# Optimization experiments

Measured on AMD Instinct MI355X. Metric: run time of the kernel, lower is better.

The kernel has to match this reference:

```python
import jax, jax.numpy as jnp
import numpy as np

W_DIM = 512
NF = 128          # n_features (all blocks equal)
NB = 4            # num_layers / n_blocks
B = 8             # batch
INIT = 32         # initial resolution: 2**(8 - 4 + 1)
IMG = 256         # 2**log_resolution
EPS = 1e-8


def setup_inputs() -> dict:
    key = jax.random.key(0)
    ks = jax.random.split(key, 12)
    d = {}
    d["w"] = jax.random.normal(ks[0], (NB, B, W_DIM), jnp.float32)
    for i in range(NB):
        r = INIT * (2 ** i)
        d[f"noise{i}"] = jax.random.normal(ks[1 + i], (2, B, 1, r, r), jnp.float32)
    # learned parameters
    d["initial_constant"] = jax.random.normal(ks[5], (1, NF, INIT, INIT), jnp.float32)
    d["to_style_w"] = jax.random.normal(ks[6], (NB, NF, W_DIM), jnp.float32)      # EqualizedLinear weights
    d["to_style_b"] = 0.1 * jax.random.normal(ks[7], (NB, NF), jnp.float32)
    d["conv_w"] = jax.random.normal(ks[8], (NB, 2, NF, NF, 3, 3), jnp.float32)    # two StyleBlock convs per block
    d["scale_noise"] = 0.1 * jax.random.normal(ks[9], (NB, 2), jnp.float32)
    d["style_bias"] = 0.1 * jax.random.normal(ks[10], (NB, 2, NF), jnp.float32)
    d["rgb_w"] = jax.random.normal(ks[11], (NB, 1, NF, 1, 1), jnp.float32)        # ToRGB 1x1 convs
    return d


def _resize(x, h, w):
    # bilinear, half-pixel centers (matches F.interpolate align_corners=False)
    return jax.image.resize(x, (x.shape[0], x.shape[1], h, w), "bilinear")


def _mod_conv(x, s, weight, demodulate):
    # x: [B, Cin, H, W], s: [B, Cin], weight: [Cout, Cin, k, k]
    out_c, in_c, k, _ = weight.shape
    c = 1.0 / np.sqrt(in_c * k * k)  # EqualizedWeight scale
    ws = (weight * c)[None] * s[:, None, :, None, None]  # [B, Cout, Cin, k, k]
    if demodulate:
        ws = ws * jax.lax.rsqrt(jnp.sum(ws * ws, axis=(2, 3, 4), keepdims=True) + EPS)
    conv = lambda xi, wi: jax.lax.conv_general_dilated(xi[None], wi, (1, 1), "SAME")[0]
    return jax.vmap(conv)(x, ws)  # per-sample weights == grouped conv with groups=B


def _style_block(x, s, wconv, sn, b, noise):
    x = _mod_conv(x, s, wconv, True)
    x = x + sn * noise
    return jax.nn.leaky_relu(x + b[None, :, None, None], 0.2)


def reference(w, noise0, noise1, noise2, noise3, initial_constant, to_style_w,
              to_style_b, conv_w, scale_noise, style_bias, rgb_w):
    noises = [noise0, noise1, noise2, noise3]
    b = w.shape[1]
    x = jax.nn.relu(jnp.broadcast_to(initial_constant, (b,) + initial_constant.shape[1:]))
    cl = 1.0 / np.sqrt(W_DIM)  # EqualizedLinear scale
    rgb_sum = jnp.zeros((b, 1, IMG, IMG), x.dtype)
    for i in range(NB):
        if i > 0:
            x = _resize(x, x.shape[2] * 2, x.shape[3] * 2)
        s = w[i] @ (to_style_w[i] * cl).T + to_style_b[i]  # [B, NF]
        x = _style_block(x, s, conv_w[i, 0], scale_noise[i, 0], style_bias[i, 0], noises[i][0])
        x = _style_block(x, s, conv_w[i, 1], scale_noise[i, 1], style_bias[i, 1], noises[i][1])
        rgb = _mod_conv(x, s, rgb_w[i], False)  # [B, 1, h, w]
        rgb_sum = rgb_sum + _resize(rgb, IMG, IMG)
    return rgb_sum / 2 + 0.5
```

## Files before the change

kernel.cpp:

```cpp
#include <hip/hip_runtime.h>
#include <math.h>

#define NB 4
#define BATCH 8
#define NF 128
#define WDIM 512
#define EPS_D 1e-8f

typedef unsigned short ushortT;
typedef __attribute__((ext_vector_type(8))) short short8v;
typedef __attribute__((ext_vector_type(8))) unsigned short ushort8v;
typedef __attribute__((ext_vector_type(4))) float float4v;
typedef __attribute__((ext_vector_type(4))) unsigned int uint4v;
typedef __attribute__((ext_vector_type(2))) unsigned int uint2v;

__device__ inline unsigned short f2bf(float f) {
    unsigned u = __builtin_bit_cast(unsigned, f);
    u = (u + 0x7fffu + ((u >> 16) & 1u)) >> 16;
    return (unsigned short)u;
}
__device__ inline float bf2f(unsigned short h) {
    unsigned u = ((unsigned)h) << 16;
    return __builtin_bit_cast(float, u);
}

__global__ void k_style(const float* __restrict__ w,
                        const float* __restrict__ tsw,
                        const float* __restrict__ tsb,
                        float* __restrict__ s) {
    int gid = blockIdx.x * blockDim.x + threadIdx.x;
    if (gid >= NB * BATCH * NF) return;
    int i = gid >> 10;
    int b = (gid >> 7) & 7;
    int o = gid & 127;
    const float cl = 0.044194173824159216f;
    const float* wr = w + (i * BATCH + b) * WDIM;
    const float* tr = tsw + (i * NF + o) * WDIM;
    float acc = 0.f;
    for (int k = 0; k < WDIM; ++k) acc += wr[k] * tr[k];
    s[gid] = acc * cl + tsb[i * NF + o];
}

__global__ void k_demod(const float* __restrict__ conv_w,
                        const float* __restrict__ s,
                        float* __restrict__ d) {
    int bx = blockIdx.x;
    int l = bx >> 7;
    int o = bx & 127;
    int lane = threadIdx.x;
    const float* wb = conv_w + (size_t)((l * NF + o) * NF) * 9;
    float t0 = 0.f, t1 = 0.f;
    for (int k = 0; k < 9; ++k) {
        float a = wb[lane * 9 + k];        t0 += a * a;
        float c = wb[(lane + 64) * 9 + k]; t1 += c * c;
    }
    const float c2 = 1.0f / 1152.0f;
    int i = l >> 1;
    for (int b = 0; b < BATCH; ++b) {
        float s0 = s[(i * BATCH + b) * NF + lane];
        float s1 = s[(i * BATCH + b) * NF + lane + 64];
        float v = t0 * s0 * s0 + t1 * s1 * s1;
        for (int off = 32; off > 0; off >>= 1) v += __shfl_down(v, off);
        if (lane == 0) d[(l * BATCH + b) * NF + o] = rsqrtf(v * c2 + EPS_D);
    }
}

__global__ void k_wmodF(const float* __restrict__ cw, const float* __restrict__ s,
                        ushortT* __restrict__ wm) {
    int idx = blockIdx.x * blockDim.x + threadIdx.x;
    int lane = idx & 63;
    int mf = (idx >> 6) & 7;
    int kcc = (idx >> 9) & 3;
    int t = (idx >> 11) % 9;
    int r2 = idx / (2048 * 9);
    int b = r2 & 7;
    int l = r2 >> 3;
    if (l >= 8) return;
    const float cscale = 0.029462782549439483f;
    int co = mf * 16 + (lane & 15);
    int kb = kcc * 32 + (lane >> 4) * 8;
    const float* src = cw + (((size_t)l * NF + co) * NF) * 9;
    const float* sr = s + ((l >> 1) * BATCH + b) * NF;
    ushort8v o;
    #pragma unroll
    for (int e = 0; e < 8; ++e) {
        int ci = kb + e;
        o[e] = f2bf(src[(size_t)ci * 9 + t] * cscale * sr[ci]);
    }
    *(ushort8v*)(wm + (size_t)idx * 8) = o;
}

__global__ void k_prep_init(const float* __restrict__ ic, ushortT* __restrict__ xp,
                            int total) {
    for (int idx = blockIdx.x * blockDim.x + threadIdx.x; idx < total;
         idx += gridDim.x * blockDim.x) {
        int ci = idx & 127;
        int p = (idx >> 7) & 1023;
        float v = ic[ci * 1024 + p];
        xp[idx] = f2bf(v > 0.f ? v : 0.f);
    }
}

__global__ void k_up2_bf(const ushortT* __restrict__ in, ushortT* __restrict__ out,
                         int h, int w, int total) {
    int W2 = w * 2, H2 = h * 2;
    for (int gid = blockIdx.x * blockDim.x + threadIdx.x; gid < total;
         gid += gridDim.x * blockDim.x) {
        int cg = gid & 15;
        int t = gid >> 4;
        int ox = t % W2; t /= W2;
        int oy = t % H2; int zb = t / H2;
        int y0 = (oy >> 1) - 1 + (oy & 1);
        float wy0 = (oy & 1) ? 0.75f : 0.25f;
        int x0 = (ox >> 1) - 1 + (ox & 1);
        float wx0 = (ox & 1) ? 0.75f : 0.25f;
        int y1 = min(y0 + 1, h - 1); y0 = max(y0, 0);
        int x1 = min(x0 + 1, w - 1); x0 = max(x0, 0);
        const ushortT* base = in + (size_t)zb * h * w * 128 + cg * 8;
        ushort8v v00 = *(const ushort8v*)(base + (size_t)(y0 * w + x0) * 128);
        ushort8v v01 = *(const ushort8v*)(base + (size_t)(y0 * w + x1) * 128);
        ushort8v v10 = *(const ushort8v*)(base + (size_t)(y1 * w + x0) * 128);
        ushort8v v11 = *(const ushort8v*)(base + (size_t)(y1 * w + x1) * 128);
        float wy1 = 1.f - wy0, wx1 = 1.f - wx0;
        ushort8v o;
        #pragma unroll
        for (int k = 0; k < 8; ++k) {
            float v = wy0 * (wx0 * bf2f(v00[k]) + wx1 * bf2f(v01[k]))
                    + wy1 * (wx0 * bf2f(v10[k]) + wx1 * bf2f(v11[k]));
            o[k] = f2bf(v);
        }
        *(ushort8v*)(out + ((size_t)(zb * H2 + oy) * W2 + ox) * 128 + cg * 8) = o;
    }
}

template<int NOY>
__global__ __launch_bounds__(256, 3) void k_conv7(
    const ushortT* __restrict__ xp, ushortT* __restrict__ yp,
    const ushortT* __restrict__ wF, const float* __restrict__ d_b,
    const float* __restrict__ nz, const float* __restrict__ bias,
    const float* __restrict__ sn_ptr, const float* __restrict__ s_blk,
    const float* __restrict__ rgbw_i, float* __restrict__ rgbb,
    int H, int W, int b0, int do_rgb)
{
    __shared__ __align__(16) char lb[46080];
    int tid = threadIdx.x;
    int lane = tid & 63;
    int wv = tid >> 6;
    int wm = wv & 1, wn = wv >> 1;
    int lm = lane & 15, lk = lane >> 4;
    int tilesX = W >> 4;
    int tx0 = (blockIdx.x % tilesX) << 4;
    int ty0 = (blockIdx.x / tilesX) << 3;
    int zb = blockIdx.y;
    int b = b0 + zb;

    const char* xbase = (const char*)(xp + (size_t)zb * H * W * 128);
    int offs[6];
    #pragma unroll
    for (int it = 0; it < 6; ++it) {
        int cw = it * 64 + lane;
        int off = -1;
        if (cw < 360) {
            int chunk = wv * 360 + cw;
            int px = chunk >> 3, slot = chunk & 7;
            int hy = px / 18, hx = px - hy * 18;
            int gy = ty0 + hy - 1, gx = tx0 + hx - 1;
            if ((unsigned)gy < (unsigned)H && (unsigned)gx < (unsigned)W)
                off = (gy * W + gx) * 256 + ((slot ^ (px & 7)) << 4);
        }
        offs[it] = off;
    }
    {
        const uint4v zv = {0, 0, 0, 0};
        #pragma unroll
        for (int c = 0; c < 12; ++c) {
            int idx = tid + c * 256;
            if (idx < 2880) *(uint4v*)(lb + idx * 16) = zv;
        }
    }
    __syncthreads();
    #pragma unroll
    for (int it = 0; it < 6; ++it)
        if (offs[it] >= 0)
            __builtin_amdgcn_global_load_lds(
                (const __attribute__((address_space(1))) void*)(xbase + offs[it]),
                (__attribute__((address_space(3))) void*)(lb + wv * 5760 + it * 1024), 16, 0, 0);
    __syncthreads();
    #pragma unroll
    for (int it = 0; it < 6; ++it)
        if (offs[it] >= 0)
            __builtin_amdgcn_global_load_lds(
                (const __attribute__((address_space(1))) void*)(xbase + offs[it] + 128),
                (__attribute__((address_space(3))) void*)(lb + 23040 + wv * 5760 + it * 1024), 16, 0, 0);

    float4v acc[4][4];
    #pragma unroll
    for (int mf = 0; mf < 4; ++mf)
        #pragma unroll
        for (int nf = 0; nf < 4; ++nf)
            acc[mf][nf] = (float4v){0.f, 0.f, 0.f, 0.f};

    const ushortT* wB = wF + (size_t)b * (9 * 4 * 4096);
    for (int cih = 0; cih < 2; ++cih) {
        if (cih) __syncthreads();
        const char* buf = lb + cih * 23040;
        #pragma unroll
        for (int tap = 0; tap < 9; ++tap) {
            const int dy = (tap < 3) ? 0 : (tap < 6 ? 1 : 2);
            const int dx = tap - dy * 3;
            #pragma unroll
            for (int kc = 0; kc < 2; ++kc) {
                const ushortT* ap = wB + ((size_t)(tap * 4 + cih * 2 + kc) << 12)
                                    + wm * 2048 + lane * 8;
                short8v a0 = *(const short8v*)(ap);
                short8v a1 = *(const short8v*)(ap + 512);
                short8v a2 = *(const short8v*)(ap + 1024);
                short8v a3 = *(const short8v*)(ap + 1536);
                #pragma unroll
                for (int nf = 0; nf < 4; ++nf) {
                    int row = nf * 2 + (lm >> 3) + dy;
                    int col = wn * 8 + (lm & 7) + dx;
                    int hp = row * 18 + col;
                    short8v bf = *(const short8v*)(buf + hp * 128
                                 + ((((kc << 2) + lk) ^ (hp & 7)) << 4));
                    acc[0][nf] = __builtin_amdgcn_mfma_f32_16x16x32_bf16(a0, bf, acc[0][nf], 0, 0, 0);
                    acc[1][nf] = __builtin_amdgcn_mfma_f32_16x16x32_bf16(a1, bf, acc[1][nf], 0, 0, 0);
                    acc[2][nf] = __builtin_amdgcn_mfma_f32_16x16x32_bf16(a2, bf, acc[2][nf], 0, 0, 0);
                    acc[3][nf] = __builtin_amdgcn_mfma_f32_16x16x32_bf16(a3, bf, acc[3][nf], 0, 0, 0);
                }
            }
        }
    }
    __syncthreads();

    float sn = sn_ptr[0];
    float nv[4];
    #pragma unroll
    for (int nf = 0; nf < 4; ++nf) {
        int gy = ty0 + nf * 2 + (lm >> 3);
        int gx = tx0 + wn * 8 + (lm & 7);
        nv[nf] = sn * nz[((size_t)b * H + gy) * W + gx];
    }
    const float cl2 = 0.08838834764831845f;

    if (NOY) {
        float rgbs[4] = {0.f, 0.f, 0.f, 0.f};
        #pragma unroll
        for (int mf = 0; mf < 4; ++mf) {
            int co0 = wm * 64 + mf * 16 + lk * 4;
            float4v dd = *(const float4v*)(d_b + b * 128 + co0);
            float4v bb = *(const float4v*)(bias + co0);
            float4v rw = *(const float4v*)(rgbw_i + co0);
            float4v sv = *(const float4v*)(s_blk + b * 128 + co0);
            #pragma unroll
            for (int nf = 0; nf < 4; ++nf)
                #pragma unroll
                for (int e = 0; e < 4; ++e) {
                    float t = acc[mf][nf][e] * dd[e] + nv[nf] + bb[e];
                    t = t > 0.f ? t : 0.2f * t;
                    rgbs[nf] += t * rw[e] * cl2 * sv[e];
                }
        }
        #pragma unroll
        for (int nf = 0; nf < 4; ++nf) {
            float r = rgbs[nf];
            r += __shfl_xor(r, 16, 64);
            r += __shfl_xor(r, 32, 64);
            if (lane < 16) {
                int gy = ty0 + nf * 2 + (lane >> 3);
                int gx = tx0 + wn * 8 + (lane & 7);
                rgbb[((size_t)(wm * BATCH + b) * H + gy) * W + gx] = r;
            }
        }
        return;
    }

    float rgbs[4] = {0.f, 0.f, 0.f, 0.f};
    unsigned pka[4][4][2];
    #pragma unroll
    for (int mf = 0; mf < 4; ++mf) {
        int co0 = wm * 64 + mf * 16 + lk * 4;
        float4v dd = *(const float4v*)(d_b + b * 128 + co0);
        float4v bb = *(const float4v*)(bias + co0);
        float4v cf = {0.f, 0.f, 0.f, 0.f};
        if (do_rgb) {
            float4v rw = *(const float4v*)(rgbw_i + co0);
            float4v sv = *(const float4v*)(s_blk + b * 128 + co0);
            #pragma unroll
            for (int e = 0; e < 4; ++e) cf[e] = rw[e] * cl2 * sv[e];
        }
        #pragma unroll
        for (int nf = 0; nf < 4; ++nf) {
            float v[4];
            #pragma unroll
            for (int e = 0; e < 4; ++e) {
                float t = acc[mf][nf][e] * dd[e] + nv[nf] + bb[e];
                v[e] = t > 0.f ? t : 0.2f * t;
            }
            if (do_rgb)
                rgbs[nf] += v[0] * cf[0] + v[1] * cf[1] + v[2] * cf[2] + v[3] * cf[3];
            pka[mf][nf][0] = (unsigned)f2bf(v[0]) | ((unsigned)f2bf(v[1]) << 16);
            pka[mf][nf][1] = (unsigned)f2bf(v[2]) | ((unsigned)f2bf(v[3]) << 16);
        }
    }
    if (do_rgb) {
        #pragma unroll
        for (int nf = 0; nf < 4; ++nf) {
            float r = rgbs[nf];
            r += __shfl_xor(r, 16, 64);
            r += __shfl_xor(r, 32, 64);
            if (lane < 16) {
                int gy = ty0 + nf * 2 + (lane >> 3);
                int gx = tx0 + wn * 8 + (lane & 7);
                rgbb[((size_t)(wm * BATCH + b) * H + gy) * W + gx] = r;
            }
        }
    }
    char* xb2 = (char*)(yp + (size_t)zb * H * W * 128);
    #pragma unroll
    for (int h = 0; h < 2; ++h) {
        if (wm == h) {
            #pragma unroll
            for (int mf = 0; mf < 4; ++mf) {
                int cb = (mf * 16 + lk * 4) * 2;
                #pragma unroll
                for (int nf = 0; nf < 4; ++nf) {
                    int pxl = (nf * 2 + (lm >> 3)) * 16 + wn * 8 + (lm & 7);
                    int ad = pxl * 128 + (cb ^ ((pxl & 7) << 4));
                    uint2v pk2;
                    pk2[0] = pka[mf][nf][0];
                    pk2[1] = pka[mf][nf][1];
                    *(uint2v*)(lb + ad) = pk2;
                }
            }
        }
        __syncthreads();
        for (int c = tid; c < 1024; c += 256) {
            int pxl = c >> 3, ck = c & 7;
            uint4v v = *(const uint4v*)(lb + pxl * 128 + ((ck << 4) ^ ((pxl & 7) << 4)));
            int gy = ty0 + (pxl >> 4), gx = tx0 + (pxl & 15);
            *(uint4v*)(xb2 + ((size_t)(gy * W + gx)) * 256 + h * 128 + ck * 16) = v;
        }
        if (h == 0) __syncthreads();
    }
}

__global__ __launch_bounds__(256, 2) void k_mega(
    const ushortT* __restrict__ up256,
    const ushortT* __restrict__ wm6,
    const ushortT* __restrict__ wm7,
    const float* __restrict__ d6, const float* __restrict__ d7,
    const float* __restrict__ nz6, const float* __restrict__ nz7,
    const float* __restrict__ bias6, const float* __restrict__ bias7,
    const float* __restrict__ sn6p, const float* __restrict__ sn7p,
    const float* __restrict__ s_blk, const float* __restrict__ rgbw_i,
    float* __restrict__ rgbb, int b0)
{
    __shared__ __align__(16) char lb[61440];
    const int J0 = 15360;
    int tid = threadIdx.x;
    int lane = tid & 63;
    int wv = tid >> 6;
    int wm = wv & 1, wn = wv >> 1;
    int lm = lane & 15, lk = lane >> 4;
    int tx0 = (blockIdx.x & 15) << 4;
    int ty0 = (blockIdx.x >> 4) << 3;
    int zb = blockIdx.y;
    int b = b0 + zb;

    int ib[6], prr[6], pcc[6];
    bool pv[6];
    #pragma unroll
    for (int nf = 0; nf < 6; ++nf) {
        int p = wn * 96 + nf * 16 + lm;
        pv[nf] = (p < 180);
        int pc = pv[nf] ? p : 0;
        prr[nf] = pc / 18;
        pcc[nf] = pc - prr[nf] * 18;
        ib[nf] = prr[nf] * 20 + pcc[nf];
    }

    const char* xbase = (const char*)(up256 + (size_t)zb * 256 * 256 * 128);
    int offs[4];
    #pragma unroll
    for (int k = 0; k < 4; ++k) {
        int c = tid + k * 256;
        int off = -1;
        if (c < 960) {
            int ip = c >> 2, d = c & 3;
            int iy = ip / 20, ix = ip - iy * 20;
            int oy = ty0 + iy - 2, ox = tx0 + ix - 2;
            if ((unsigned)oy < 256u && (unsigned)ox < 256u)
                off = (oy * 256 + ox) * 256 + ((d ^ ((ip >> 1) & 3)) << 4);
        }
        offs[k] = off;
    }
    {
        const uint4v zv = {0, 0, 0, 0};
        for (int c = tid; c < 960; c += 256) *(uint4v*)(lb + c * 16) = zv;
    }
    __syncthreads();

    float4v j0a[4][6];
    #pragma unroll
    for (int mf = 0; mf < 4; ++mf)
        #pragma unroll
        for (int nf = 0; nf < 6; ++nf)
            j0a[mf][nf] = (float4v){0.f, 0.f, 0.f, 0.f};

    const ushortT* wB6 = wm6 + (size_t)b * (9 * 4 * 4096);
    const ushortT* wB7 = wm7 + (size_t)b * (9 * 4 * 4096);

    for (int q = 0; q < 4; ++q) {
        __builtin_amdgcn_sched_barrier(0);
        #pragma unroll
        for (int k = 0; k < 4; ++k)
            if (offs[k] >= 0)
                __builtin_amdgcn_global_load_lds(
                    (const __attribute__((address_space(1))) void*)(xbase + offs[k] + q * 64),
                    (__attribute__((address_space(3))) void*)(lb + k * 4096 + wv * 1024), 16, 0, 0);
        asm volatile("s_waitcnt vmcnt(0)" ::: "memory");
        __builtin_amdgcn_sched_barrier(0);
        __syncthreads();
        #pragma unroll
        for (int tap = 0; tap < 9; ++tap) {
            const int dy = (tap < 3) ? 0 : (tap < 6 ? 1 : 2);
            const int dx = tap - dy * 3;
            const ushortT* ap = wB6 + ((size_t)(tap * 4 + q) << 12) + wm * 2048 + lane * 8;
            short8v a0 = *(const short8v*)(ap);
            short8v a1 = *(const short8v*)(ap + 512);
            short8v a2 = *(const short8v*)(ap + 1024);
            short8v a3 = *(const short8v*)(ap + 1536);
            #pragma unroll
            for (int nf = 0; nf < 6; ++nf) {
                int ipx = ib[nf] + dy * 20 + dx;
                short8v bf = *(const short8v*)(lb + ipx * 64
                             + ((lk ^ ((ipx >> 1) & 3)) << 4));
                j0a[0][nf] = __builtin_amdgcn_mfma_f32_16x16x32_bf16(a0, bf, j0a[0][nf], 0, 0, 0);
                j0a[1][nf] = __builtin_amdgcn_mfma_f32_16x16x32_bf16(a1, bf, j0a[1][nf], 0, 0, 0);
                j0a[2][nf] = __builtin_amdgcn_mfma_f32_16x16x32_bf16(a2, bf, j0a[2][nf], 0, 0, 0);
                j0a[3][nf] = __builtin_amdgcn_mfma_f32_16x16x32_bf16(a3, bf, j0a[3][nf], 0, 0, 0);
            }
        }
        __builtin_amdgcn_sched_barrier(0);
        __syncthreads();
        __builtin_amdgcn_sched_barrier(0);
    }

    {
        float sn6 = sn6p[0];
        #pragma unroll
        for (int nf = 0; nf < 6; ++nf) {
            if (!pv[nf]) continue;
            int p = wn * 96 + nf * 16 + lm;
            int oy = ty0 + prr[nf] - 1, ox = tx0 + pcc[nf] - 1;
            bool inimg = ((unsigned)oy < 256u) && ((unsigned)ox < 256u);
            float nv = inimg ? sn6 * nz6[((size_t)b * 256 + oy) * 256 + ox] : 0.f;
            #pragma unroll
            for (int mf = 0; mf < 4; ++mf) {
                int co0 = wm * 64 + mf * 16 + lk * 4;
                uint2v pk2 = {0u, 0u};
                if (inimg) {
                    float4v dd = *(const float4v*)(d6 + b * 128 + co0);
                    float4v bb = *(const float4v*)(bias6 + co0);
                    float v[4];
                    #pragma unroll
                    for (int e = 0; e < 4; ++e) {
                        float t = j0a[mf][nf][e] * dd[e] + nv + bb[e];
                        v[e] = t > 0.f ? t : 0.2f * t;
                    }
                    pk2[0] = (unsigned)f2bf(v[0]) | ((unsigned)f2bf(v[1]) << 16);
                    pk2[1] = (unsigned)f2bf(v[2]) | ((unsigned)f2bf(v[3]) << 16);
                }
                int ad = p * 256 + ((co0 * 2) ^ ((p & 7) << 4));
                *(uint2v*)(lb + J0 + ad) = pk2;
            }
        }
    }
    __syncthreads();

    float4v acc[4][4];
    #pragma unroll
    for (int mf = 0; mf < 4; ++mf)
        #pragma unroll
        for (int nf = 0; nf < 4; ++nf)
            acc[mf][nf] = (float4v){0.f, 0.f, 0.f, 0.f};

    #pragma unroll
    for (int tap = 0; tap < 9; ++tap) {
        const int dy = (tap < 3) ? 0 : (tap < 6 ? 1 : 2);
        const int dx = tap - dy * 3;
        #pragma unroll
        for (int kcc = 0; kcc < 4; ++kcc) {
            const ushortT* ap = wB7 + ((size_t)(tap * 4 + kcc) << 12) + wm * 2048 + lane * 8;
            short8v a0 = *(const short8v*)(ap);
            short8v a1 = *(const short8v*)(ap + 512);
            short8v a2 = *(const short8v*)(ap + 1024);
            short8v a3 = *(const short8v*)(ap + 1536);
            #pragma unroll
            for (int nf = 0; nf < 4; ++nf) {
                int row = nf * 2 + (lm >> 3) + dy;
                int col = wn * 8 + (lm & 7) + dx;
                int hp = row * 18 + col;
                short8v bf = *(const short8v*)(lb + J0 + hp * 256
                             + ((kcc * 64 + lk * 16) ^ ((hp & 7) << 4)));
                acc[0][nf] = __builtin_amdgcn_mfma_f32_16x16x32_bf16(a0, bf, acc[0][nf], 0, 0, 0);
                acc[1][nf] = __builtin_amdgcn_mfma_f32_16x16x32_bf16(a1, bf, acc[1][nf], 0, 0, 0);
                acc[2][nf] = __builtin_amdgcn_mfma_f32_16x16x32_bf16(a2, bf, acc[2][nf], 0, 0, 0);
                acc[3][nf] = __builtin_amdgcn_mfma_f32_16x16x32_bf16(a3, bf, acc[3][nf], 0, 0, 0);
            }
        }
    }

    float sn7 = sn7p[0];
    float nv7[4];
    #pragma unroll
    for (int nf = 0; nf < 4; ++nf) {
        int gy = ty0 + nf * 2 + (lm >> 3);
        int gx = tx0 + wn * 8 + (lm & 7);
        nv7[nf] = sn7 * nz7[((size_t)b * 256 + gy) * 256 + gx];
    }
    const float cl2 = 0.08838834764831845f;
    float rgbs[4] = {0.f, 0.f, 0.f, 0.f};
    #pragma unroll
    for (int mf = 0; mf < 4; ++mf) {
        int co0 = wm * 64 + mf * 16 + lk * 4;
        float4v dd = *(const float4v*)(d7 + b * 128 + co0);
        float4v bb = *(const float4v*)(bias7 + co0);
        float4v rw = *(const float4v*)(rgbw_i + co0);
        float4v sv = *(const float4v*)(s_blk + b * 128 + co0);
        #pragma unroll
        for (int nf = 0; nf < 4; ++nf)
            #pragma unroll
            for (int e = 0; e < 4; ++e) {
                float t = acc[mf][nf][e] * dd[e] + nv7[nf] + bb[e];
                t = t > 0.f ? t : 0.2f * t;
                rgbs[nf] += t * rw[e] * cl2 * sv[e];
            }
    }
    #pragma unroll
    for (int nf = 0; nf < 4; ++nf) {
        float r = rgbs[nf];
        r += __shfl_xor(r, 16, 64);
        r += __shfl_xor(r, 32, 64);
        if (lane < 16) {
            int gy = ty0 + nf * 2 + (lane >> 3);
            int gx = tx0 + wn * 8 + (lane & 7);
            rgbb[((size_t)(wm * BATCH + b) * 256 + gy) * 256 + gx] = r;
        }
    }
}

__global__ void k_rgbacc(const float* __restrict__ rgb, float* __restrict__ acc,
                         int r, int beta, int b0, int g) {
    int idx = blockIdx.x * blockDim.x + threadIdx.x;
    if (idx >= g * 256 * 256) return;
    int ox = idx & 255;
    int oy = (idx >> 8) & 255;
    int b = b0 + (idx >> 16);
    float scale = (float)r * (1.0f / 256.0f);
    float fy = (oy + 0.5f) * scale - 0.5f;
    float fx = (ox + 0.5f) * scale - 0.5f;
    int y0 = (int)floorf(fy); float wy = fy - (float)y0;
    int x0 = (int)floorf(fx); float wx = fx - (float)x0;
    int y1 = min(y0 + 1, r - 1); y0 = max(y0, 0);
    int x1 = min(x0 + 1, r - 1); x0 = max(x0, 0);
    const float* p0 = rgb + (size_t)b * r * r;
    const float* p1 = rgb + (size_t)(BATCH + b) * r * r;
    float v00 = p0[y0 * r + x0] + p1[y0 * r + x0];
    float v01 = p0[y0 * r + x1] + p1[y0 * r + x1];
    float v10 = p0[y1 * r + x0] + p1[y1 * r + x0];
    float v11 = p0[y1 * r + x1] + p1[y1 * r + x1];
    float v = (1.f - wy) * ((1.f - wx) * v00 + wx * v01)
            +        wy  * ((1.f - wx) * v10 + wx * v11);
    int oidx = (b << 16) | (oy << 8) | ox;
    acc[oidx] = (beta ? acc[oidx] : 0.f) + v;
}

__global__ void k_final(float* __restrict__ out, int total) {
    int idx = blockIdx.x * blockDim.x + threadIdx.x;
    if (idx < total) out[idx] = out[idx] * 0.5f + 0.5f;
}

extern "C" void kernel_launch(void* const* d_in, const int* in_sizes, int n_in,
                              void* d_out, int out_size, void* d_ws, size_t ws_size,
                              hipStream_t stream) {
    const float* w     = (const float*)d_in[0];
    const float* noise[4] = {(const float*)d_in[1], (const float*)d_in[2],
                             (const float*)d_in[3], (const float*)d_in[4]};
    const float* ic    = (const float*)d_in[5];
    const float* tsw   = (const float*)d_in[6];
    const float* tsb   = (const float*)d_in[7];
    const float* cw    = (const float*)d_in[8];
    const float* snp   = (const float*)d_in[9];
    const float* sbias = (const float*)d_in[10];
    const float* rgbw  = (const float*)d_in[11];

    const size_t WM_BYTES = 8ull * 8 * 9 * 4 * 8 * 64 * 8 * 2;
    const size_t RGBB = 2ull * BATCH * 65536 * 4;
    const size_t FIXED = 16384 + 32768 + RGBB + WM_BYTES;
    const size_t PER_S = 65536ull * 128 * 2;
    int g = 0;
    for (int cand = 8; cand >= 1; cand >>= 1)
        if (ws_size >= FIXED + 2ull * cand * PER_S) { g = cand; break; }
    if (g == 0) return;

    char* ws = (char*)d_ws;
    float* s_all   = (float*)ws;
    float* d_all   = (float*)(ws + 16384);
    float* rgbb    = (float*)(ws + 49152);
    ushortT* wmall = (ushortT*)(ws + 49152 + RGBB);
    ushortT* bufA  = (ushortT*)(ws + FIXED);
    ushortT* bufB  = (ushortT*)(ws + FIXED + (size_t)g * PER_S);
    float* accb    = (float*)d_out;

    k_style<<<64, 64, 0, stream>>>(w, tsw, tsb, s_all);
    k_demod<<<1024, 64, 0, stream>>>(cw, s_all, d_all);
    k_wmodF<<<4608, 256, 0, stream>>>(cw, s_all, wmall);

    #define CONV(T2, SRC, DST, L, R, B0, G, RGB) do {                          \
        dim3 grid(((R) / 16) * ((R) / 8), (G));                                \
        k_conv7<T2><<<grid, 256, 0, stream>>>((SRC), (DST),                    \
            wmall + (size_t)(L) * (8 * 9 * 4 * 4096), d_all + (L) * BATCH * NF,\
            noise[(L) >> 1] + (size_t)((L) & 1) * BATCH * (R) * (R),           \
            sbias + (L) * NF, snp + (L), s_all + ((L) >> 1) * BATCH * NF,      \
            rgbw + ((L) >> 1) * NF, rgbb, (R), (R), (B0), (RGB));              \
    } while (0)

    if (g >= 2) {
        ushortT* xb = bufA;
        ushortT* tb = bufB;
        k_prep_init<<<4096, 256, 0, stream>>>(ic, xb, BATCH * 1024 * 128);
        for (int i = 0; i < 3; ++i) {
            int r = 32 << i;
            if (i > 0) {
                int total = BATCH * r * r * 16;
                int blocks = (total + 255) / 256;
                if (blocks > 2048) blocks = 2048;
                k_up2_bf<<<blocks, 256, 0, stream>>>(xb, tb, r / 2, r / 2, total);
                ushortT* t2 = xb; xb = tb; tb = t2;
            }
            CONV(0, xb, tb, i * 2 + 0, r, 0, BATCH, 0);
            { ushortT* t2 = xb; xb = tb; tb = t2; }
            CONV(0, xb, tb, i * 2 + 1, r, 0, BATCH, 1);
            { ushortT* t2 = xb; xb = tb; tb = t2; }
            int tot = BATCH * 256 * 256;
            k_rgbacc<<<(tot + 255) / 256, 256, 0, stream>>>(rgbb, accb, r, i > 0, 0, BATCH);
        }
        for (int b0 = 0; b0 < BATCH; b0 += g) {
            int total = g * 256 * 256 * 16;
            k_up2_bf<<<2048, 256, 0, stream>>>(xb + (size_t)b0 * 2097152, tb,
                                               128, 128, total);
            dim3 mgrid(512, g);
            k_mega<<<mgrid, 256, 0, stream>>>(tb,
                wmall + 6ull * (8 * 9 * 4 * 4096), wmall + 7ull * (8 * 9 * 4 * 4096),
                d_all + 6 * BATCH * NF, d_all + 7 * BATCH * NF,
                noise[3], noise[3] + (size_t)BATCH * 65536,
                sbias + 6 * NF, sbias + 7 * NF, snp + 6, snp + 7,
                s_all + 3 * BATCH * NF, rgbw + 3 * NF, rgbb, b0);
        }
        int tot = BATCH * 256 * 256;
        k_rgbacc<<<(tot + 255) / 256, 256, 0, stream>>>(rgbb, accb, 256, 1, 0, BATCH);
    } else {
        for (int b0 = 0; b0 < BATCH; ++b0) {
            ushortT* xb = bufA;
            ushortT* tb = bufB;
            k_prep_init<<<1024, 256, 0, stream>>>(ic, xb, 1024 * 128);
            for (int i = 0; i < NB; ++i) {
                int r = 32 << i;
                if (i > 0) {
                    int total = r * r * 16;
                    int blocks = (total + 255) / 256;
                    if (blocks > 2048) blocks = 2048;
                    k_up2_bf<<<blocks, 256, 0, stream>>>(xb, tb, r / 2, r / 2, total);
                    ushortT* t2 = xb; xb = tb; tb = t2;
                }
                CONV(0, xb, tb, i * 2 + 0, r, b0, 1, 0);
                { ushortT* t2 = xb; xb = tb; tb = t2; }
                if (i < 3) {
                    CONV(0, xb, tb, i * 2 + 1, r, b0, 1, 1);
                    { ushortT* t2 = xb; xb = tb; tb = t2; }
                } else {
                    CONV(1, xb, tb, 7, r, b0, 1, 1);
                }
                int tot = 1 * 256 * 256;
                k_rgbacc<<<(tot + 255) / 256, 256, 0, stream>>>(rgbb, accb, r, i > 0, b0, 1);
            }
        }
    }
    #undef CONV
    k_final<<<(out_size + 255) / 256, 256, 0, stream>>>(accb, out_size);
}
```

Before: 769.1 us.

## Double-buffer input channel chunks and split intermediate into two channel halves in LDS

The first conv's input channel quarters are now loaded into two alternating LDS buffers, so the next chunk's global-to-LDS load is issued before the current chunk's MFMAs instead of stalling on each load. To fit the second buffer, the intermediate activation tile is stored in two 64-channel halves, each written by one wave group and consumed by the second conv in turn. This adds syncs but keeps LDS at 53760 bytes, which still allows two blocks per CU. The extra syncs and the serialized half-writes may offset part of the overlap gain.

```diff
diff --git a/kernel.cpp b/kernel.cpp
--- a/kernel.cpp
+++ b/kernel.cpp
@@ -347,8 +347,7 @@
 
 __global__ __launch_bounds__(256, 2) void k_mega(
     const ushortT* __restrict__ up256,
-    const ushortT* __restrict__ wm6,
-    const ushortT* __restrict__ wm7,
+    const ushortT* __restrict__ wm6, const ushortT* __restrict__ wm7,
     const float* __restrict__ d6, const float* __restrict__ d7,
     const float* __restrict__ nz6, const float* __restrict__ nz7,
     const float* __restrict__ bias6, const float* __restrict__ bias7,
@@ -356,8 +355,8 @@
     const float* __restrict__ s_blk, const float* __restrict__ rgbw_i,
     float* __restrict__ rgbb, int b0)
 {
-    __shared__ __align__(16) char lb[61440];
-    const int J0 = 15360;
+    __shared__ __align__(16) char lb[53760];
+    const int QB = 15360, J0 = 30720;
     int tid = threadIdx.x;
     int lane = tid & 63;
     int wv = tid >> 6;
@@ -397,7 +396,7 @@
     }
     {
         const uint4v zv = {0, 0, 0, 0};
-        for (int c = tid; c < 960; c += 256) *(uint4v*)(lb + c * 16) = zv;
+        for (int c = tid; c < 1920; c += 256) *(uint4v*)(lb + c * 16) = zv;
     }
     __syncthreads();
 
@@ -411,17 +410,25 @@
     const ushortT* wB6 = wm6 + (size_t)b * (9 * 4 * 4096);
     const ushortT* wB7 = wm7 + (size_t)b * (9 * 4 * 4096);
 
+    #define MISSUE(q, buf) do { \
+        __builtin_amdgcn_sched_barrier(0); \
+        _Pragma("unroll") \
+        for (int k = 0; k < 4; ++k) \
+            if (offs[k] >= 0) \
+                __builtin_amdgcn_global_load_lds( \
+                    (const __attribute__((address_space(1))) void*)(xbase + offs[k] + (q) * 64), \
+                    (__attribute__((address_space(3))) void*)(lb + (buf) * QB + k * 4096 + wv * 1024), 16, 0, 0); \
+        __builtin_amdgcn_sched_barrier(0); \
+    } while (0)
+
+    MISSUE(0, 0);
+    asm volatile("s_waitcnt vmcnt(0)" ::: "memory");
+    __builtin_amdgcn_sched_barrier(0);
+    __syncthreads();
+
     for (int q = 0; q < 4; ++q) {
-        __builtin_amdgcn_sched_barrier(0);
-        #pragma unroll
-        for (int k = 0; k < 4; ++k)
-            if (offs[k] >= 0)
-                __builtin_amdgcn_global_load_lds(
-                    (const __attribute__((address_space(1))) void*)(xbase + offs[k] + q * 64),
-                    (__attribute__((address_space(3))) void*)(lb + k * 4096 + wv * 1024), 16, 0, 0);
-        asm volatile("s_waitcnt vmcnt(0)" ::: "memory");
-        __builtin_amdgcn_sched_barrier(0);
-        __syncthreads();
+        if (q < 3) MISSUE(q + 1, (q + 1) & 1);
+        const char* qb = lb + (q & 1) * QB;
         #pragma unroll
         for (int tap = 0; tap < 9; ++tap) {
             const int dy = (tap < 3) ? 0 : (tap < 6 ? 1 : 2);
@@ -434,7 +441,7 @@
             #pragma unroll
             for (int nf = 0; nf < 6; ++nf) {
                 int ipx = ib[nf] + dy * 20 + dx;
-                short8v bf = *(const short8v*)(lb + ipx * 64
+                short8v bf = *(const short8v*)(qb + ipx * 64
                              + ((lk ^ ((ipx >> 1) & 3)) << 4));
                 j0a[0][nf] = __builtin_amdgcn_mfma_f32_16x16x32_bf16(a0, bf, j0a[0][nf], 0, 0, 0);
                 j0a[1][nf] = __builtin_amdgcn_mfma_f32_16x16x32_bf16(a1, bf, j0a[1][nf], 0, 0, 0);
@@ -442,42 +449,11 @@
                 j0a[3][nf] = __builtin_amdgcn_mfma_f32_16x16x32_bf16(a3, bf, j0a[3][nf], 0, 0, 0);
             }
         }
+        asm volatile("s_waitcnt vmcnt(0)" ::: "memory");
         __builtin_amdgcn_sched_barrier(0);
         __syncthreads();
-        __builtin_amdgcn_sched_barrier(0);
-    }
-
-    {
-        float sn6 = sn6p[0];
-        #pragma unroll
-        for (int nf = 0; nf < 6; ++nf) {
-            if (!pv[nf]) continue;
-            int p = wn * 96 + nf * 16 + lm;
-            int oy = ty0 + prr[nf] - 1, ox = tx0 + pcc[nf] - 1;
-            bool inimg = ((unsigned)oy < 256u) && ((unsigned)ox < 256u);
-            float nv = inimg ? sn6 * nz6[((size_t)b * 256 + oy) * 256 + ox] : 0.f;
-            #pragma unroll
-            for (int mf = 0; mf < 4; ++mf) {
-                int co0 = wm * 64 + mf * 16 + lk * 4;
-                uint2v pk2 = {0u, 0u};
-                if (inimg) {
-                    float4v dd = *(const float4v*)(d6 + b * 128 + co0);
-                    float4v bb = *(const float4v*)(bias6 + co0);
-                    float v[4];
-                    #pragma unroll
-                    for (int e = 0; e < 4; ++e) {
-                        float t = j0a[mf][nf][e] * dd[e] + nv + bb[e];
-                        v[e] = t > 0.f ? t : 0.2f * t;
-                    }
-                    pk2[0] = (unsigned)f2bf(v[0]) | ((unsigned)f2bf(v[1]) << 16);
-                    pk2[1] = (unsigned)f2bf(v[2]) | ((unsigned)f2bf(v[3]) << 16);
-                }
-                int ad = p * 256 + ((co0 * 2) ^ ((p & 7) << 4));
-                *(uint2v*)(lb + J0 + ad) = pk2;
-            }
-        }
-    }
-    __syncthreads();
+    }
+    #undef MISSUE
 
     float4v acc[4][4];
     #pragma unroll
@@ -486,28 +462,64 @@
         for (int nf = 0; nf < 4; ++nf)
             acc[mf][nf] = (float4v){0.f, 0.f, 0.f, 0.f};
 
-    #pragma unroll
-    for (int tap = 0; tap < 9; ++tap) {
-        const int dy = (tap < 3) ? 0 : (tap < 6 ? 1 : 2);
-        const int dx = tap - dy * 3;
-        #pragma unroll
-        for (int kcc = 0; kcc < 4; ++kcc) {
-            const ushortT* ap = wB7 + ((size_t)(tap * 4 + kcc) << 12) + wm * 2048 + lane * 8;
-            short8v a0 = *(const short8v*)(ap);
-            short8v a1 = *(const short8v*)(ap + 512);
-            short8v a2 = *(const short8v*)(ap + 1024);
-            short8v a3 = *(const short8v*)(ap + 1536);
-            #pragma unroll
-            for (int nf = 0; nf < 4; ++nf) {
-                int row = nf * 2 + (lm >> 3) + dy;
-                int col = wn * 8 + (lm & 7) + dx;
-                int hp = row * 18 + col;
-                short8v bf = *(const short8v*)(lb + J0 + hp * 256
-                             + ((kcc * 64 + lk * 16) ^ ((hp & 7) << 4)));
-                acc[0][nf] = __builtin_amdgcn_mfma_f32_16x16x32_bf16(a0, bf, acc[0][nf], 0, 0, 0);
-                acc[1][nf] = __builtin_amdgcn_mfma_f32_16x16x32_bf16(a1, bf, acc[1][nf], 0, 0, 0);
-                acc[2][nf] = __builtin_amdgcn_mfma_f32_16x16x32_bf16(a2, bf, acc[2][nf], 0, 0, 0);
-                acc[3][nf] = __builtin_amdgcn_mfma_f32_16x16x32_bf16(a3, bf, acc[3][nf], 0, 0, 0);
+    float sn6 = sn6p[0];
+    #pragma unroll
+    for (int h = 0; h < 2; ++h) {
+        if (h) __syncthreads();
+        if (wm == h) {
+            #pragma unroll
+            for (int nf = 0; nf < 6; ++nf) {
+                if (!pv[nf]) continue;
+                int p = wn * 96 + nf * 16 + lm;
+                int oy = ty0 + prr[nf] - 1, ox = tx0 + pcc[nf] - 1;
+                bool inimg = ((unsigned)oy < 256u) && ((unsigned)ox < 256u);
+                float nv = inimg ? sn6 * nz6[((size_t)b * 256 + oy) * 256 + ox] : 0.f;
+                #pragma unroll
+                for (int mf = 0; mf < 4; ++mf) {
+                    int col = mf * 16 + lk * 4;
+                    uint2v pk2 = {0u, 0u};
+                    if (inimg) {
+                        float4v dd = *(const float4v*)(d6 + b * 128 + wm * 64 + col);
+                        float4v bb = *(const float4v*)(bias6 + wm * 64 + col);
+                        float v[4];
+                        #pragma unroll
+                        for (int e = 0; e < 4; ++e) {
+                            float t = j0a[mf][nf][e] * dd[e] + nv + bb[e];
+                            v[e] = t > 0.f ? t : 0.2f * t;
+                        }
+                        pk2[0] = (unsigned)f2bf(v[0]) | ((unsigned)f2bf(v[1]) << 16);
+                        pk2[1] = (unsigned)f2bf(v[2]) | ((unsigned)f2bf(v[3]) << 16);
+                    }
+                    int ad = p * 128 + ((col * 2) ^ ((p & 7) << 4));
+                    *(uint2v*)(lb + J0 + ad) = pk2;
+                }
+            }
+        }
+        __syncthreads();
+        #pragma unroll
+        for (int tap = 0; tap < 9; ++tap) {
+            const int dy = (tap < 3) ? 0 : (tap < 6 ? 1 : 2);
+            const int dx = tap - dy * 3;
+            #pragma unroll
+            for (int kc = 0; kc < 2; ++kc) {
+                const ushortT* ap = wB7 + ((size_t)(tap * 4 + 2 * h + kc) << 12)
+                                    + wm * 2048 + lane * 8;
+                short8v a0 = *(const short8v*)(ap);
+                short8v a1 = *(const short8v*)(ap + 512);
+                short8v a2 = *(const short8v*)(ap + 1024);
+                short8v a3 = *(const short8v*)(ap + 1536);
+                #pragma unroll
+                for (int nf = 0; nf < 4; ++nf) {
+                    int row = nf * 2 + (lm >> 3) + dy;
+                    int col = wn * 8 + (lm & 7) + dx;
+                    int hp = row * 18 + col;
+                    short8v bf = *(const short8v*)(lb + J0 + hp * 128
+                                 + ((kc * 64 + lk * 16) ^ ((hp & 7) << 4)));
+                    acc[0][nf] = __builtin_amdgcn_mfma_f32_16x16x32_bf16(a0, bf, acc[0][nf], 0, 0, 0);
+                    acc[1][nf] = __builtin_amdgcn_mfma_f32_16x16x32_bf16(a1, bf, acc[1][nf], 0, 0, 0);
+                    acc[2][nf] = __builtin_amdgcn_mfma_f32_16x16x32_bf16(a2, bf, acc[2][nf], 0, 0, 0);
+                    acc[3][nf] = __builtin_amdgcn_mfma_f32_16x16x32_bf16(a3, bf, acc[3][nf], 0, 0, 0);
+                }
             }
         }
     }
```

New measurement: 1.043 ms. +35.6%, slower.
